# Kernel optimization log

Hardware: AMD Instinct MI355X
Metric: run time of the kernel (lower is better)

The kernel has to match this reference:

```python
import jax, jax.numpy as jnp
import numpy as np


def setup_inputs() -> dict:
    key = jax.random.key(0)
    kq, kk, kv = jax.random.split(key, 3)
    B, H, S, D = 2, 8, 2048, 64
    Q = jax.random.normal(kq, (B, H, S, D), dtype=jnp.float32)
    K = jax.random.normal(kk, (B, 1, S, D), dtype=jnp.float32)
    V = jax.random.normal(kv, (B, 1, S, D), dtype=jnp.float32)
    return {"Q": Q, "K": K, "V": V}


def reference(Q, K, V):
    # Multi-query attention: K/V have a single shared head.
    D = Q.shape[-1]
    scale = 1.0 / jnp.sqrt(jnp.asarray(D, dtype=Q.dtype))
    Kh = K[:, 0]  # [B, S, D]
    Vh = V[:, 0]  # [B, S, D]
    # scores: [B, H, Sq, Sk]
    scores = jnp.einsum('bhqd,bkd->bhqk', Q, Kh) * scale
    probs = jax.nn.softmax(scores, axis=-1)
    out = jnp.einsum('bhqk,bkd->bhqd', probs, Vh)  # [B, H, S, D]
    return out
```

## Files before the change

### kernel.cpp

```cpp
#include <hip/hip_runtime.h>
#include <hip/hip_bf16.h>
#include <stdint.h>

typedef __attribute__((ext_vector_type(8)))  short    bf16x8;
typedef __attribute__((ext_vector_type(16))) float    f32x16;
typedef __attribute__((ext_vector_type(2)))  float    f32x2;
typedef __attribute__((ext_vector_type(4)))  float    float4v;
typedef __attribute__((ext_vector_type(4)))  unsigned uint4v;
typedef __attribute__((ext_vector_type(2)))  int      int2v;

#define DEVINL static __device__ __forceinline__

#define B_  2
#define H_  8
#define S_  2048
#define D_  64
#define KVB 128
#define NKT (S_ / KVB)

DEVINL unsigned short f2bf(float f) {
  union { float f; unsigned u; } v; v.f = f;
  unsigned r = v.u + 0x7FFFu + ((v.u >> 16) & 1u);
  return (unsigned short)(r >> 16);
}

DEVINL unsigned short bfu(float f) {
  __hip_bfloat16 h = __float2bfloat16(f);
  unsigned short u; __builtin_memcpy(&u, &h, 2); return u;
}

DEVINL unsigned pkcvt(float a, float b) {
  return (unsigned)bfu(a) | ((unsigned)bfu(b) << 16);
}

DEVINL void gload_lds16(const void* g, void* l) {
  __builtin_amdgcn_global_load_lds(
      (const __attribute__((address_space(1))) void*)g,
      (__attribute__((address_space(3))) void*)l, 16, 0, 0);
}

DEVINL bf16x8 frag_from_words(unsigned a, unsigned b, unsigned c, unsigned d) {
  union { unsigned u[4]; bf16x8 v; } x;
  x.u[0] = a; x.u[1] = b; x.u[2] = c; x.u[3] = d;
  return x.v;
}

#define CROW(r, hi) (((r) & 3) + 8 * ((r) >> 2) + 4 * (hi))

__global__ __launch_bounds__(256) void prep_kernel(
    const float* __restrict__ K, const float* __restrict__ V,
    unsigned short* __restrict__ KVf) {
  const int blk = blockIdx.x;
  const int b  = blk >> 5;
  const int kt = (blk >> 1) & 15;
  const int t  = threadIdx.x;
  const int w  = t >> 6, l = t & 63;
  const int lq = l & 31, hi = l >> 5;

  unsigned short* out = KVf + (size_t)(b * 16 + kt) * 16384;

  if ((blk & 1) == 0) {
#pragma unroll
    for (int j = 0; j < 4; ++j) {
      const int fi = w * 4 + j;
      const int kh = fi >> 2, ks = fi & 3;
      const float* src = K + ((size_t)(b * 2048 + kt * 128 + kh * 32 + lq)) * 64 + ks * 16 + hi * 8;
      const float4v x0 = *(const float4v*)(src);
      const float4v x1 = *(const float4v*)(src + 4);
      uint4v o;
      o.x = (unsigned)f2bf(x0.x) | ((unsigned)f2bf(x0.y) << 16);
      o.y = (unsigned)f2bf(x0.z) | ((unsigned)f2bf(x0.w) << 16);
      o.z = (unsigned)f2bf(x1.x) | ((unsigned)f2bf(x1.y) << 16);
      o.w = (unsigned)f2bf(x1.z) | ((unsigned)f2bf(x1.w) << 16);
      *(uint4v*)(out + fi * 512 + l * 8) = o;
    }
  } else {
    __shared__ float Vs[128][65];
#pragma unroll
    for (int rep = 0; rep < 4; ++rep) {
      const int row = rep * 32 + (t >> 3);
      const int col = (t & 7) * 8;
      const float* src = V + ((size_t)(b * 2048 + kt * 128 + row)) * 64 + col;
      const float4v y0 = *(const float4v*)(src);
      const float4v y1 = *(const float4v*)(src + 4);
      Vs[row][col + 0] = y0.x; Vs[row][col + 1] = y0.y;
      Vs[row][col + 2] = y0.z; Vs[row][col + 3] = y0.w;
      Vs[row][col + 4] = y1.x; Vs[row][col + 5] = y1.y;
      Vs[row][col + 6] = y1.z; Vs[row][col + 7] = y1.w;
    }
    __syncthreads();
#pragma unroll
    for (int j = 0; j < 4; ++j) {
      const int fj = w * 4 + j;
      const int kh = fj >> 2, s = (fj >> 1) & 1, nt = fj & 1;
      const int d  = nt * 32 + lq;
      const int k0 = kh * 32 + s * 16 + hi * 8;
      unsigned short o[8];
#pragma unroll
      for (int e = 0; e < 8; ++e) o[e] = f2bf(Vs[k0 + e][d]);
      uint4v wv;
      wv.x = (unsigned)o[0] | ((unsigned)o[1] << 16);
      wv.y = (unsigned)o[2] | ((unsigned)o[3] << 16);
      wv.z = (unsigned)o[4] | ((unsigned)o[5] << 16);
      wv.w = (unsigned)o[6] | ((unsigned)o[7] << 16);
      *(uint4v*)(out + (16 + fj) * 512 + l * 8) = wv;
    }
  }
}

__global__ __launch_bounds__(512, 4) void attn_kernel(
    const float* __restrict__ Q, const unsigned short* __restrict__ KVf,
    float* __restrict__ O) {
  __shared__ __align__(16) unsigned char smem[65536];

  const int bid = blockIdx.x;
  const int b  = bid >> 8;
  const int h  = (bid >> 5) & 7;
  const int qt = bid & 31;

  const int tid  = threadIdx.x;
  const int lane = tid & 63;
  const int wave = tid >> 6;
  const int qg   = wave & 1;
  const int kh   = wave >> 1;
  const int hi   = lane >> 5;
  const int lq   = lane & 31;

  const unsigned char* kp = (const unsigned char*)KVf + (size_t)b * 16 * 32768;

  const float qscale = 0.125f * 1.4426950408889634f;
  const float* qrow = Q + ((size_t)((b * H_ + h) * S_) + (size_t)(qt * 64 + qg * 32 + lq)) * 64;
  bf16x8 qfrag[4];
#pragma unroll
  for (int ks = 0; ks < 4; ++ks) {
    const float* p = qrow + ks * 16 + hi * 8;
    float4v x0 = *(const float4v*)(p);
    float4v x1 = *(const float4v*)(p + 4);
    bf16x8 f;
    f[0] = (short)f2bf(x0.x * qscale); f[1] = (short)f2bf(x0.y * qscale);
    f[2] = (short)f2bf(x0.z * qscale); f[3] = (short)f2bf(x0.w * qscale);
    f[4] = (short)f2bf(x1.x * qscale); f[5] = (short)f2bf(x1.y * qscale);
    f[6] = (short)f2bf(x1.z * qscale); f[7] = (short)f2bf(x1.w * qscale);
    qfrag[ks] = f;
  }

  f32x16 acc0, acc1;
#pragma unroll
  for (int r = 0; r < 16; ++r) { acc0[r] = 0.f; acc1[r] = 0.f; }
  float mrun = -__builtin_inff();
  float lrun = 0.f;

#define STAGE(BUF)                                                        \
  do {                                                                    \
    _Pragma("unroll")                                                     \
    for (int j = 0; j < 4; ++j)                                           \
      gload_lds16(kp + j * 8192 + tid * 16,                               \
                  smem + (BUF) * 32768 + j * 8192 + tid * 16);            \
    kp += 32768;                                                          \
  } while (0)

  STAGE(0);

  int buf = 0;
  for (int kt = 0; kt < NKT; ++kt) {
    __syncthreads();

    if (kt + 1 < NKT) STAGE(buf ^ 1);

    const unsigned short* Kt = (const unsigned short*)(smem + buf * 32768) + kh * 2048;
    f32x16 c;
#pragma unroll
    for (int r = 0; r < 16; ++r) c[r] = 0.f;
    __builtin_amdgcn_s_setprio(1);
#pragma unroll
    for (int ks = 0; ks < 4; ++ks) {
      const bf16x8 a = *(const bf16x8*)(Kt + ks * 512 + lane * 8);
      c = __builtin_amdgcn_mfma_f32_32x32x16_bf16(a, qfrag[ks], c, 0, 0, 0);
    }
    __builtin_amdgcn_s_setprio(0);

    f32x2 m2 = (f32x2){c[0], c[1]};
#pragma unroll
    for (int r = 1; r < 8; ++r)
      m2 = __builtin_elementwise_max(m2, (f32x2){c[2 * r], c[2 * r + 1]});
    float mx = fmaxf(m2.x, m2.y);
    mx = fmaxf(mx, __shfl_xor(mx, 32));

    if (!__all(mx <= mrun + 8.f)) {
      const float mnew = fmaxf(mrun, mx);
      const float fac  = __builtin_amdgcn_exp2f(mrun - mnew);
#pragma unroll
      for (int r = 0; r < 16; ++r) {
        const float fr = __shfl(fac, CROW(r, hi));
        acc0[r] *= fr; acc1[r] *= fr;
      }
      lrun *= fac;
      mrun = mnew;
    }

#pragma unroll
    for (int r = 0; r < 16; ++r) c[r] = __builtin_amdgcn_exp2f(c[r] - mrun);
    f32x2 ps = (f32x2){0.f, 0.f};
#pragma unroll
    for (int r = 0; r < 8; ++r) ps += (f32x2){c[2 * r], c[2 * r + 1]};
    float psum = ps.x + ps.y;
    psum += __shfl_xor(psum, 32);
    lrun += psum;

    const unsigned short* Vt = (const unsigned short*)(smem + buf * 32768) + 8192 + kh * 2048;
#pragma unroll
    for (int s = 0; s < 2; ++s) {
      const unsigned wx0 = pkcvt(c[8 * s + 0], c[8 * s + 1]);
      const unsigned wx1 = pkcvt(c[8 * s + 2], c[8 * s + 3]);
      const unsigned wy0 = pkcvt(c[8 * s + 4], c[8 * s + 5]);
      const unsigned wy1 = pkcvt(c[8 * s + 6], c[8 * s + 7]);
      const int2v s02 = __builtin_amdgcn_permlane32_swap((int)wx0, (int)wy0, false, false);
      const int2v s13 = __builtin_amdgcn_permlane32_swap((int)wx1, (int)wy1, false, false);
      const bf16x8 pfrag = frag_from_words((unsigned)s02.x, (unsigned)s13.x,
                                           (unsigned)s02.y, (unsigned)s13.y);
      __builtin_amdgcn_s_setprio(1);
      const bf16x8 bv0 = *(const bf16x8*)(Vt + (s * 2 + 0) * 512 + lane * 8);
      acc0 = __builtin_amdgcn_mfma_f32_32x32x16_bf16(pfrag, bv0, acc0, 0, 0, 0);
      const bf16x8 bv1 = *(const bf16x8*)(Vt + (s * 2 + 1) * 512 + lane * 8);
      acc1 = __builtin_amdgcn_mfma_f32_32x32x16_bf16(pfrag, bv1, acc1, 0, 0, 0);
      __builtin_amdgcn_s_setprio(0);
    }

    buf ^= 1;
  }

  __syncthreads();
  float* Mb = (float*)smem;
  float* Lb = Mb + 256;
  float* Ab = Mb + 512;
  if (lane < 32) {
    Mb[(qg * 4 + kh) * 32 + lane] = mrun;
    Lb[(qg * 4 + kh) * 32 + lane] = lrun;
  }
  __syncthreads();
  const float m0_ = Mb[(qg * 4 + 0) * 32 + lq], l0_ = Lb[(qg * 4 + 0) * 32 + lq];
  const float m1_ = Mb[(qg * 4 + 1) * 32 + lq], l1_ = Lb[(qg * 4 + 1) * 32 + lq];
  const float m2_ = Mb[(qg * 4 + 2) * 32 + lq], l2_ = Lb[(qg * 4 + 2) * 32 + lq];
  const float m3_ = Mb[(qg * 4 + 3) * 32 + lq], l3_ = Lb[(qg * 4 + 3) * 32 + lq];
  const float mtot = fmaxf(fmaxf(m0_, m1_), fmaxf(m2_, m3_));
  const float ltot = l0_ * __builtin_amdgcn_exp2f(m0_ - mtot)
                   + l1_ * __builtin_amdgcn_exp2f(m1_ - mtot)
                   + l2_ * __builtin_amdgcn_exp2f(m2_ - mtot)
                   + l3_ * __builtin_amdgcn_exp2f(m3_ - mtot);
  const float sself = __builtin_amdgcn_exp2f(mrun - mtot);

  if (kh > 0) {
    float* dst = Ab + (size_t)(qg * 3 + (kh - 1)) * 2048;
#pragma unroll
    for (int r = 0; r < 16; ++r) {
      const float sr = __shfl(sself, CROW(r, hi));
      dst[CROW(r, hi) * 64 + lq]      = acc0[r] * sr;
      dst[CROW(r, hi) * 64 + 32 + lq] = acc1[r] * sr;
    }
  }
  __syncthreads();
  if (kh == 0) {
    const float linv = 1.f / ltot;
    const float* a0 = Ab + (size_t)(qg * 3 + 0) * 2048;
    const float* a1 = Ab + (size_t)(qg * 3 + 1) * 2048;
    const float* a2 = Ab + (size_t)(qg * 3 + 2) * 2048;
    float* obase = O + ((size_t)((b * H_ + h) * S_) + (size_t)(qt * 64 + qg * 32)) * 64;
#pragma unroll
    for (int r = 0; r < 16; ++r) {
      const float sr = __shfl(sself, CROW(r, hi));
      const float iv = __shfl(linv,  CROW(r, hi));
      const int row  = CROW(r, hi);
      obase[(size_t)row * 64 + lq] =
          (acc0[r] * sr + a0[row * 64 + lq] + a1[row * 64 + lq] + a2[row * 64 + lq]) * iv;
      obase[(size_t)row * 64 + 32 + lq] =
          (acc1[r] * sr + a0[row * 64 + 32 + lq] + a1[row * 64 + 32 + lq] + a2[row * 64 + 32 + lq]) * iv;
    }
  }
}

extern "C" void kernel_launch(void* const* d_in, const int* in_sizes, int n_in,
                              void* d_out, int out_size, void* d_ws, size_t ws_size,
                              hipStream_t stream) {
  const float* Q = (const float*)d_in[0];
  const float* K = (const float*)d_in[1];
  const float* V = (const float*)d_in[2];
  float* O = (float*)d_out;

  unsigned short* KVf = (unsigned short*)d_ws;

  prep_kernel<<<64, 256, 0, stream>>>(K, V, KVf);
  attn_kernel<<<B_ * H_ * (S_ / 64), 512, 0, stream>>>(Q, KVf, O);
}
```

Baseline: 43.33 us.

## Load K/V fragments directly from global into registers, dropping LDS staging

Replaces the double-buffered global-to-LDS staging and per-tile __syncthreads with direct per-lane global loads of K and V MFMA fragments into registers. K for the next tile is prefetched into a ping-pong register set while the current tile computes, and the loop is unrolled by two. This removes block-wide barriers and LDS traffic, and shrinks shared memory to what the final cross-wave reduction needs. In exchange, the two waves that share each fragment (qg 0 and 1) now each load it from global/L2, and register pressure rises.

Result: slower. 56.90 us (+31.3%).

```diff
diff --git a/kernel.cpp b/kernel.cpp
--- a/kernel.cpp
+++ b/kernel.cpp
@@ -31,12 +31,6 @@
 
 DEVINL unsigned pkcvt(float a, float b) {
   return (unsigned)bfu(a) | ((unsigned)bfu(b) << 16);
-}
-
-DEVINL void gload_lds16(const void* g, void* l) {
-  __builtin_amdgcn_global_load_lds(
-      (const __attribute__((address_space(1))) void*)g,
-      (__attribute__((address_space(3))) void*)l, 16, 0, 0);
 }
 
 DEVINL bf16x8 frag_from_words(unsigned a, unsigned b, unsigned c, unsigned d) {
@@ -111,7 +105,7 @@
 __global__ __launch_bounds__(512, 4) void attn_kernel(
     const float* __restrict__ Q, const unsigned short* __restrict__ KVf,
     float* __restrict__ O) {
-  __shared__ __align__(16) unsigned char smem[65536];
+  __shared__ __align__(16) float smem_f[12800];
 
   const int bid = blockIdx.x;
   const int b  = bid >> 8;
@@ -126,7 +120,8 @@
   const int hi   = lane >> 5;
   const int lq   = lane & 31;
 
-  const unsigned char* kp = (const unsigned char*)KVf + (size_t)b * 16 * 32768;
+  const unsigned char* tb = (const unsigned char*)KVf
+      + (size_t)b * 16 * 32768 + (size_t)kh * 4096 + (size_t)lane * 16;
 
   const float qscale = 0.125f * 1.4426950408889634f;
   const float* qrow = Q + ((size_t)((b * H_ + h) * S_) + (size_t)(qt * 64 + qg * 32 + lq)) * 64;
@@ -150,89 +145,99 @@
   float mrun = -__builtin_inff();
   float lrun = 0.f;
 
-#define STAGE(BUF)                                                        \
-  do {                                                                    \
-    _Pragma("unroll")                                                     \
-    for (int j = 0; j < 4; ++j)                                           \
-      gload_lds16(kp + j * 8192 + tid * 16,                               \
-                  smem + (BUF) * 32768 + j * 8192 + tid * 16);            \
-    kp += 32768;                                                          \
+#define BODY(KC0, KC1, KC2, KC3, KN0, KN1, KN2, KN3, KT)                               \
+  do {                                                                                 \
+    const unsigned char* vb_ = tb + 16384 + (size_t)(KT) * 32768;                      \
+    const bf16x8 v0_ = *(const bf16x8*)(vb_);                                          \
+    const bf16x8 v1_ = *(const bf16x8*)(vb_ + 1024);                                   \
+    const bf16x8 v2_ = *(const bf16x8*)(vb_ + 2048);                                   \
+    const bf16x8 v3_ = *(const bf16x8*)(vb_ + 3072);                                   \
+    f32x16 c;                                                                          \
+    _Pragma("unroll") for (int r = 0; r < 16; ++r) c[r] = 0.f;                         \
+    __builtin_amdgcn_s_setprio(1);                                                     \
+    c = __builtin_amdgcn_mfma_f32_32x32x16_bf16(KC0, qfrag[0], c, 0, 0, 0);            \
+    c = __builtin_amdgcn_mfma_f32_32x32x16_bf16(KC1, qfrag[1], c, 0, 0, 0);            \
+    c = __builtin_amdgcn_mfma_f32_32x32x16_bf16(KC2, qfrag[2], c, 0, 0, 0);            \
+    c = __builtin_amdgcn_mfma_f32_32x32x16_bf16(KC3, qfrag[3], c, 0, 0, 0);            \
+    __builtin_amdgcn_s_setprio(0);                                                     \
+    if ((KT) + 1 < NKT) {                                                              \
+      const unsigned char* kb_ = tb + (size_t)((KT) + 1) * 32768;                      \
+      KN0 = *(const bf16x8*)(kb_);                                                     \
+      KN1 = *(const bf16x8*)(kb_ + 1024);                                              \
+      KN2 = *(const bf16x8*)(kb_ + 2048);                                              \
+      KN3 = *(const bf16x8*)(kb_ + 3072);                                              \
+    }                                                                                  \
+    f32x2 m2 = (f32x2){c[0], c[1]};                                                    \
+    _Pragma("unroll") for (int r = 1; r < 8; ++r)                                      \
+      m2 = __builtin_elementwise_max(m2, (f32x2){c[2 * r], c[2 * r + 1]});             \
+    float mx = fmaxf(m2.x, m2.y);                                                      \
+    mx = fmaxf(mx, __shfl_xor(mx, 32));                                                \
+    if (!__all(mx <= mrun + 8.f)) {                                                    \
+      const float mnew = fmaxf(mrun, mx);                                              \
+      const float fac  = __builtin_amdgcn_exp2f(mrun - mnew);                          \
+      _Pragma("unroll") for (int r = 0; r < 16; ++r) {                                 \
+        const float fr = __shfl(fac, CROW(r, hi));                                     \
+        acc0[r] *= fr; acc1[r] *= fr;                                                  \
+      }                                                                                \
+      lrun *= fac;                                                                     \
+      mrun = mnew;                                                                     \
+    }                                                                                  \
+    _Pragma("unroll") for (int r = 0; r < 16; ++r)                                     \
+      c[r] = __builtin_amdgcn_exp2f(c[r] - mrun);                                      \
+    f32x2 ps = (f32x2){0.f, 0.f};                                                      \
+    _Pragma("unroll") for (int r = 0; r < 8; ++r)                                      \
+      ps += (f32x2){c[2 * r], c[2 * r + 1]};                                           \
+    float psum = ps.x + ps.y;                                                          \
+    psum += __shfl_xor(psum, 32);                                                      \
+    lrun += psum;                                                                      \
+    {                                                                                  \
+      const unsigned wx0 = pkcvt(c[0], c[1]);                                          \
+      const unsigned wx1 = pkcvt(c[2], c[3]);                                          \
+      const unsigned wy0 = pkcvt(c[4], c[5]);                                          \
+      const unsigned wy1 = pkcvt(c[6], c[7]);                                          \
+      const int2v s02 = __builtin_amdgcn_permlane32_swap((int)wx0, (int)wy0, false, false); \
+      const int2v s13 = __builtin_amdgcn_permlane32_swap((int)wx1, (int)wy1, false, false); \
+      const bf16x8 pfrag = frag_from_words((unsigned)s02.x, (unsigned)s13.x,           \
+                                           (unsigned)s02.y, (unsigned)s13.y);          \
+      __builtin_amdgcn_s_setprio(1);                                                   \
+      acc0 = __builtin_amdgcn_mfma_f32_32x32x16_bf16(pfrag, v0_, acc0, 0, 0, 0);       \
+      acc1 = __builtin_amdgcn_mfma_f32_32x32x16_bf16(pfrag, v1_, acc1, 0, 0, 0);       \
+      __builtin_amdgcn_s_setprio(0);                                                   \
+    }                                                                                  \
+    {                                                                                  \
+      const unsigned wx0 = pkcvt(c[8], c[9]);                                          \
+      const unsigned wx1 = pkcvt(c[10], c[11]);                                        \
+      const unsigned wy0 = pkcvt(c[12], c[13]);                                        \
+      const unsigned wy1 = pkcvt(c[14], c[15]);                                        \
+      const int2v s02 = __builtin_amdgcn_permlane32_swap((int)wx0, (int)wy0, false, false); \
+      const int2v s13 = __builtin_amdgcn_permlane32_swap((int)wx1, (int)wy1, false, false); \
+      const bf16x8 pfrag = frag_from_words((unsigned)s02.x, (unsigned)s13.x,           \
+                                           (unsigned)s02.y, (unsigned)s13.y);          \
+      __builtin_amdgcn_s_setprio(1);                                                   \
+      acc0 = __builtin_amdgcn_mfma_f32_32x32x16_bf16(pfrag, v2_, acc0, 0, 0, 0);       \
+      acc1 = __builtin_amdgcn_mfma_f32_32x32x16_bf16(pfrag, v3_, acc1, 0, 0, 0);       \
+      __builtin_amdgcn_s_setprio(0);                                                   \
+    }                                                                                  \
   } while (0)
 
-  STAGE(0);
-
-  int buf = 0;
-  for (int kt = 0; kt < NKT; ++kt) {
-    __syncthreads();
-
-    if (kt + 1 < NKT) STAGE(buf ^ 1);
-
-    const unsigned short* Kt = (const unsigned short*)(smem + buf * 32768) + kh * 2048;
-    f32x16 c;
-#pragma unroll
-    for (int r = 0; r < 16; ++r) c[r] = 0.f;
-    __builtin_amdgcn_s_setprio(1);
-#pragma unroll
-    for (int ks = 0; ks < 4; ++ks) {
-      const bf16x8 a = *(const bf16x8*)(Kt + ks * 512 + lane * 8);
-      c = __builtin_amdgcn_mfma_f32_32x32x16_bf16(a, qfrag[ks], c, 0, 0, 0);
-    }
-    __builtin_amdgcn_s_setprio(0);
-
-    f32x2 m2 = (f32x2){c[0], c[1]};
-#pragma unroll
-    for (int r = 1; r < 8; ++r)
-      m2 = __builtin_elementwise_max(m2, (f32x2){c[2 * r], c[2 * r + 1]});
-    float mx = fmaxf(m2.x, m2.y);
-    mx = fmaxf(mx, __shfl_xor(mx, 32));
-
-    if (!__all(mx <= mrun + 8.f)) {
-      const float mnew = fmaxf(mrun, mx);
-      const float fac  = __builtin_amdgcn_exp2f(mrun - mnew);
-#pragma unroll
-      for (int r = 0; r < 16; ++r) {
-        const float fr = __shfl(fac, CROW(r, hi));
-        acc0[r] *= fr; acc1[r] *= fr;
-      }
-      lrun *= fac;
-      mrun = mnew;
-    }
-
-#pragma unroll
-    for (int r = 0; r < 16; ++r) c[r] = __builtin_amdgcn_exp2f(c[r] - mrun);
-    f32x2 ps = (f32x2){0.f, 0.f};
-#pragma unroll
-    for (int r = 0; r < 8; ++r) ps += (f32x2){c[2 * r], c[2 * r + 1]};
-    float psum = ps.x + ps.y;
-    psum += __shfl_xor(psum, 32);
-    lrun += psum;
-
-    const unsigned short* Vt = (const unsigned short*)(smem + buf * 32768) + 8192 + kh * 2048;
-#pragma unroll
-    for (int s = 0; s < 2; ++s) {
-      const unsigned wx0 = pkcvt(c[8 * s + 0], c[8 * s + 1]);
-      const unsigned wx1 = pkcvt(c[8 * s + 2], c[8 * s + 3]);
-      const unsigned wy0 = pkcvt(c[8 * s + 4], c[8 * s + 5]);
-      const unsigned wy1 = pkcvt(c[8 * s + 6], c[8 * s + 7]);
-      const int2v s02 = __builtin_amdgcn_permlane32_swap((int)wx0, (int)wy0, false, false);
-      const int2v s13 = __builtin_amdgcn_permlane32_swap((int)wx1, (int)wy1, false, false);
-      const bf16x8 pfrag = frag_from_words((unsigned)s02.x, (unsigned)s13.x,
-                                           (unsigned)s02.y, (unsigned)s13.y);
-      __builtin_amdgcn_s_setprio(1);
-      const bf16x8 bv0 = *(const bf16x8*)(Vt + (s * 2 + 0) * 512 + lane * 8);
-      acc0 = __builtin_amdgcn_mfma_f32_32x32x16_bf16(pfrag, bv0, acc0, 0, 0, 0);
-      const bf16x8 bv1 = *(const bf16x8*)(Vt + (s * 2 + 1) * 512 + lane * 8);
-      acc1 = __builtin_amdgcn_mfma_f32_32x32x16_bf16(pfrag, bv1, acc1, 0, 0, 0);
-      __builtin_amdgcn_s_setprio(0);
-    }
-
-    buf ^= 1;
-  }
-
+  bf16x8 ka0, ka1, ka2, ka3, kb0, kb1, kb2, kb3;
+  {
+    const unsigned char* k0_ = tb;
+    ka0 = *(const bf16x8*)(k0_);
+    ka1 = *(const bf16x8*)(k0_ + 1024);
+    ka2 = *(const bf16x8*)(k0_ + 2048);
+    ka3 = *(const bf16x8*)(k0_ + 3072);
+  }
+
+  for (int kt = 0; kt < NKT; kt += 2) {
+    BODY(ka0, ka1, ka2, ka3, kb0, kb1, kb2, kb3, kt);
+    BODY(kb0, kb1, kb2, kb3, ka0, ka1, ka2, ka3, kt + 1);
+  }
+
+  float* Mb = smem_f;
+  float* Lb = smem_f + 256;
+  float* Ab = smem_f + 512;
   __syncthreads();
-  float* Mb = (float*)smem;
-  float* Lb = Mb + 256;
-  float* Ab = Mb + 512;
   if (lane < 32) {
     Mb[(qg * 4 + kh) * 32 + lane] = mrun;
     Lb[(qg * 4 + kh) * 32 + lane] = lrun;
```
